# Performance work log

Hardware: AMD Instinct MI355X
Metric: run time of the kernel (lower is better)

Reference implementation:

```python
import jax, jax.numpy as jnp
import numpy as np

N_NODES = 100000
D_IN = 256
D_OUT = 128
N_EDGES = 1600000


def setup_inputs() -> dict:
    key = jax.random.key(0)
    k1, k2, k3, k4 = jax.random.split(key, 4)
    x = jax.random.normal(k1, (N_NODES, D_IN), dtype=jnp.float32)
    edge_index = jax.random.randint(k2, (2, N_EDGES), 0, N_NODES, dtype=jnp.int64)
    # GCNConv parameters (glorot-style scale)
    W = jax.random.normal(k3, (D_IN, D_OUT), dtype=jnp.float32) * (1.0 / np.sqrt(D_IN))
    b = jax.random.normal(k4, (D_OUT,), dtype=jnp.float32) * 0.01
    return {"x": x, "edge_index": edge_index, "W": W, "b": b}


def reference(x, edge_index, W, b):
    n = x.shape[0]
    # add self-loops (PyG GCNConv default)
    loop = jnp.arange(n, dtype=edge_index.dtype)
    src = jnp.concatenate([edge_index[0], loop])
    dst = jnp.concatenate([edge_index[1], loop])
    # symmetric normalization: deg^-1/2[src] * deg^-1/2[dst]
    ones = jnp.ones(src.shape[0], dtype=x.dtype)
    deg = jax.ops.segment_sum(ones, dst, num_segments=n)
    dinv = jnp.where(deg > 0, jax.lax.rsqrt(deg), 0.0)
    norm = dinv[src] * dinv[dst]  # [E+N]
    # linear transform at nodes, then gather-scale-scatter over edges
    h = x @ W  # [N, d_out]
    msg = h[src] * norm[:, None]  # [E+N, d_out]
    out = jax.ops.segment_sum(msg, dst, num_segments=n) + b
    # CRD.forward: relu then dropout (identity in eval mode)
    return jax.nn.relu(out)
```

## Files before the change

kernel.cpp:

```cpp
#include <hip/hip_runtime.h>
#include <stdint.h>

#define D_IN 256
#define D_OUT 128
#define MAXB 800
#define NCHUNK 256

typedef __attribute__((ext_vector_type(8))) short bf16x8;
typedef __attribute__((ext_vector_type(4))) float f32x4;

__device__ __forceinline__ unsigned short f2bf(float f) {
  union { float f; uint32_t u; } v; v.f = f;
  uint32_t u = v.u;
  uint32_t r = (u + 0x7FFFu + ((u >> 16) & 1u)) >> 16;
  return (unsigned short)r;
}
__device__ __forceinline__ float bf_lo(uint32_t u) {
  union { uint32_t u; float f; } v; v.u = u << 16; return v.f;
}
__device__ __forceinline__ float bf_hi(uint32_t u) {
  union { uint32_t u; float f; } v; v.u = u & 0xFFFF0000u; return v.f;
}

__global__ __launch_bounds__(256) void k_conv_w(const float* __restrict__ W,
                                                unsigned short* __restrict__ wt) {
  int idx = blockIdx.x * 256 + threadIdx.x;
  int n = idx >> 8;
  int k = idx & 255;
  wt[idx] = f2bf(W[k * D_OUT + n]);
}

__global__ __launch_bounds__(512) void k_gemm(const float* __restrict__ x,
                                              const unsigned short* __restrict__ wt,
                                              unsigned short* __restrict__ hp, int N) {
  int wave = threadIdx.x >> 6;
  int lane = threadIdx.x & 63;
  int m = lane & 15;
  int q = lane >> 4;

  bf16x8 bw[8];
  const unsigned short* wrow = wt + (size_t)(wave * 16 + m) * D_IN + q * 8;
#pragma unroll
  for (int kt = 0; kt < 8; ++kt)
    bw[kt] = *reinterpret_cast<const bf16x8*>(wrow + kt * 32);

  int tiles = (N + 15) >> 4;
  for (int t = blockIdx.x; t < tiles; t += gridDim.x) {
    int r0 = t * 16;
    const float* xrow = x + (size_t)(r0 + m) * D_IN + q * 8;

    f32x4 acc = {0.f, 0.f, 0.f, 0.f};
#pragma unroll
    for (int kt = 0; kt < 8; ++kt) {
      float4 u0 = *reinterpret_cast<const float4*>(xrow + kt * 32);
      float4 u1 = *reinterpret_cast<const float4*>(xrow + kt * 32 + 4);
      bf16x8 av;
      av[0] = (short)f2bf(u0.x); av[1] = (short)f2bf(u0.y);
      av[2] = (short)f2bf(u0.z); av[3] = (short)f2bf(u0.w);
      av[4] = (short)f2bf(u1.x); av[5] = (short)f2bf(u1.y);
      av[6] = (short)f2bf(u1.z); av[7] = (short)f2bf(u1.w);
      acc = __builtin_amdgcn_mfma_f32_16x16x32_bf16(av, bw[kt], acc, 0, 0, 0);
    }
#pragma unroll
    for (int r = 0; r < 4; ++r) {
      int row = r0 + q * 4 + r;
      hp[(size_t)row * D_OUT + wave * 16 + m] = f2bf(acc[r]);
    }
  }
}

__global__ __launch_bounds__(256) void k_passA(const int* __restrict__ ei, int E, int CH,
                                               int NB, int* __restrict__ cntm) {
  __shared__ int bins[MAXB];
  int c = blockIdx.x;
  for (int b = threadIdx.x; b < NB; b += 256) bins[b] = 0;
  __syncthreads();
  int start = c * CH, end = min(E, start + CH);
  for (int eb = start + (int)threadIdx.x * 4; eb < end; eb += 1024) {
    int kmax = end - eb; if (kmax > 4) kmax = 4;
    if (kmax == 4) {
      int4 v = *reinterpret_cast<const int4*>(ei + E + eb);
      atomicAdd(&bins[v.x >> 7], 1);
      atomicAdd(&bins[v.y >> 7], 1);
      atomicAdd(&bins[v.z >> 7], 1);
      atomicAdd(&bins[v.w >> 7], 1);
    } else {
      for (int k = 0; k < kmax; ++k) atomicAdd(&bins[ei[E + eb + k] >> 7], 1);
    }
  }
  __syncthreads();
  for (int b = threadIdx.x; b < NB; b += 256) cntm[(size_t)b * NCHUNK + c] = bins[b];
}

__global__ __launch_bounds__(NCHUNK) void k_scanB1(const int* __restrict__ cntm,
                                                   int* __restrict__ ofs,
                                                   int* __restrict__ tot) {
  __shared__ int sc[NCHUNK];
  int b = blockIdx.x, t = threadIdx.x;
  int v = cntm[(size_t)b * NCHUNK + t];
  sc[t] = v;
  __syncthreads();
  for (int off = 1; off < NCHUNK; off <<= 1) {
    int val = (t >= off) ? sc[t - off] : 0;
    __syncthreads();
    sc[t] += val;
    __syncthreads();
  }
  ofs[(size_t)b * NCHUNK + t] = sc[t] - v;
  if (t == NCHUNK - 1) tot[b] = sc[t];
}

__global__ __launch_bounds__(256) void k_scanB2(const int* __restrict__ tot,
                                                int* __restrict__ base, int NB,
                                                int* __restrict__ nptr, int N, int E) {
  __shared__ int sc[256];
  int t = threadIdx.x;
  int v[4];
  int s = 0;
#pragma unroll
  for (int j = 0; j < 4; ++j) {
    int i = t * 4 + j;
    v[j] = (i < NB) ? tot[i] : 0;
    s += v[j];
  }
  sc[t] = s;
  __syncthreads();
  for (int off = 1; off < 256; off <<= 1) {
    int val = (t >= off) ? sc[t - off] : 0;
    __syncthreads();
    sc[t] += val;
    __syncthreads();
  }
  int ex = sc[t] - s;
#pragma unroll
  for (int j = 0; j < 4; ++j) {
    int i = t * 4 + j;
    if (i < NB) base[i] = ex;
    ex += v[j];
  }
  if (t == 0) nptr[N] = E;
}

__global__ __launch_bounds__(256) void k_passC(const int* __restrict__ ei, int E, int CH,
                                               int NB, const int* __restrict__ ofs,
                                               const int* __restrict__ base,
                                               int* __restrict__ P) {
  __shared__ int cur[MAXB];
  int c = blockIdx.x;
  for (int b = threadIdx.x; b < NB; b += 256)
    cur[b] = base[b] + ofs[(size_t)b * NCHUNK + c];
  __syncthreads();
  int start = c * CH, end = min(E, start + CH);
  for (int eb = start + (int)threadIdx.x * 4; eb < end; eb += 1024) {
    int kmax = end - eb; if (kmax > 4) kmax = 4;
    int s4[4], d4[4];
    if (kmax == 4) {
      int4 vs = *reinterpret_cast<const int4*>(ei + eb);
      int4 vd = *reinterpret_cast<const int4*>(ei + E + eb);
      s4[0] = vs.x; s4[1] = vs.y; s4[2] = vs.z; s4[3] = vs.w;
      d4[0] = vd.x; d4[1] = vd.y; d4[2] = vd.z; d4[3] = vd.w;
    } else {
      for (int k = 0; k < kmax; ++k) { s4[k] = ei[eb + k]; d4[k] = ei[E + eb + k]; }
    }
#pragma unroll
    for (int k = 0; k < 4; ++k) {
      if (k >= kmax) break;
      int d = d4[k];
      int p = atomicAdd(&cur[d >> 7], 1);
      P[p] = s4[k] | ((d & 127) << 17);
    }
  }
}

__global__ __launch_bounds__(256) void k_sortd(const int* __restrict__ P,
                                               const int* __restrict__ base,
                                               const int* __restrict__ tot,
                                               int* __restrict__ nptr,
                                               float* __restrict__ dinv,
                                               int* __restrict__ P2, int N) {
  __shared__ int ideg[128];
  __shared__ int sc[128];
  __shared__ int cur[128];
  int b = blockIdx.x, t = threadIdx.x;
  if (t < 128) ideg[t] = 0;
  __syncthreads();
  int s0 = base[b], T = tot[b];
  for (int i = s0 + t; i < s0 + T; i += 256) atomicAdd(&ideg[P[i] >> 17], 1);
  __syncthreads();
  if (t < 128) sc[t] = ideg[t];
  __syncthreads();
  for (int off = 1; off < 128; off <<= 1) {
    int v = (t < 128 && t >= off) ? sc[t - off] : 0;
    __syncthreads();
    if (t < 128) sc[t] += v;
    __syncthreads();
  }
  if (t < 128) {
    int exc = s0 + sc[t] - ideg[t];
    int node = b * 128 + t;
    if (node < N) {
      nptr[node] = exc;
      dinv[node] = rsqrtf(1.0f + (float)ideg[t]);
    }
    cur[t] = exc;
  }
  __syncthreads();
  for (int i = s0 + t; i < s0 + T; i += 256) {
    int pk = P[i];
    int p = atomicAdd(&cur[pk >> 17], 1);
    P2[p] = pk & 0x1FFFF;
  }
}

__global__ __launch_bounds__(256) void k_agg(const int* __restrict__ P2,
                                             const int* __restrict__ nptr,
                                             const uint4* __restrict__ hrows,
                                             const float* __restrict__ dinv,
                                             const float* __restrict__ bias,
                                             float* __restrict__ out, int N) {
  int wave = threadIdx.x >> 6, lane = threadIdx.x & 63;
  int node = blockIdx.x * 4 + wave;
  if (node >= N) return;
  int rs = nptr[node], re = nptr[node + 1];
  int j = lane >> 4, c = lane & 15;

  float acc[8];
#pragma unroll
  for (int k = 0; k < 8; ++k) acc[k] = 0.f;

  for (int e = rs + j; e < re; e += 4) {
    int src = P2[e];
    float r = dinv[src];
    uint4 u = hrows[(size_t)src * 16 + c];
    acc[0] += r * bf_lo(u.x); acc[1] += r * bf_hi(u.x);
    acc[2] += r * bf_lo(u.y); acc[3] += r * bf_hi(u.y);
    acc[4] += r * bf_lo(u.z); acc[5] += r * bf_hi(u.z);
    acc[6] += r * bf_lo(u.w); acc[7] += r * bf_hi(u.w);
  }
#pragma unroll
  for (int k = 0; k < 8; ++k) {
    acc[k] += __shfl_xor(acc[k], 16);
    acc[k] += __shfl_xor(acc[k], 32);
  }
  if (j == 0) {
    float rsn = dinv[node];
    uint4 uh = hrows[(size_t)node * 16 + c];
    float self[8] = {bf_lo(uh.x), bf_hi(uh.x), bf_lo(uh.y), bf_hi(uh.y),
                     bf_lo(uh.z), bf_hi(uh.z), bf_lo(uh.w), bf_hi(uh.w)};
    const float4* b4 = reinterpret_cast<const float4*>(bias);
    float4 b0 = b4[c * 2], b1 = b4[c * 2 + 1];
    float bb[8] = {b0.x, b0.y, b0.z, b0.w, b1.x, b1.y, b1.z, b1.w};
    float o[8];
#pragma unroll
    for (int k = 0; k < 8; ++k) {
      float v = rsn * (acc[k] + rsn * self[k]) + bb[k];
      o[k] = v > 0.f ? v : 0.f;
    }
    float4* orow = reinterpret_cast<float4*>(out + (size_t)node * D_OUT + c * 8);
    orow[0] = float4{o[0], o[1], o[2], o[3]};
    orow[1] = float4{o[4], o[5], o[6], o[7]};
  }
}

extern "C" void kernel_launch(void* const* d_in, const int* in_sizes, int n_in,
                              void* d_out, int out_size, void* d_ws, size_t ws_size,
                              hipStream_t stream) {
  const float* x = (const float*)d_in[0];
  const int* ei = (const int*)d_in[1];
  const float* W = (const float*)d_in[2];
  const float* bias = (const float*)d_in[3];
  int N = in_sizes[0] / D_IN;
  int E = in_sizes[1] / 2;
  float* out = (float*)d_out;

  int NB = (N + 127) >> 7;
  int CH = ((E + NCHUNK - 1) / NCHUNK + 3) & ~3;

  char* w = (char*)d_ws;
  size_t off = 0;
  auto alloc = [&](size_t bytes) -> void* {
    void* p = w + off;
    off = (off + bytes + 255) & ~(size_t)255;
    return p;
  };
  unsigned short* wt = (unsigned short*)alloc((size_t)D_IN * D_OUT * 2);
  unsigned short* hp = (unsigned short*)alloc((size_t)N * D_OUT * 2);
  float* dinv = (float*)alloc((size_t)N * 4);
  int* cntm = (int*)alloc((size_t)NB * NCHUNK * 4);
  int* ofs = (int*)alloc((size_t)NB * NCHUNK * 4);
  int* tot = (int*)alloc((size_t)NB * 4);
  int* base = (int*)alloc((size_t)NB * 4);
  int* nptr = (int*)alloc((size_t)(N + 1) * 4);
  int* P = (int*)alloc((size_t)E * 4);
  int* P2 = (int*)alloc((size_t)E * 4);
  (void)ws_size; (void)n_in; (void)out_size;

  int tiles = (N + 15) >> 4;
  int gblocks = tiles < 512 ? tiles : 512;

  k_conv_w<<<(D_IN * D_OUT) / 256, 256, 0, stream>>>(W, wt);
  k_gemm<<<gblocks, 512, 0, stream>>>(x, wt, hp, N);
  k_passA<<<NCHUNK, 256, 0, stream>>>(ei, E, CH, NB, cntm);
  k_scanB1<<<NB, NCHUNK, 0, stream>>>(cntm, ofs, tot);
  k_scanB2<<<1, 256, 0, stream>>>(tot, base, NB, nptr, N, E);
  k_passC<<<NCHUNK, 256, 0, stream>>>(ei, E, CH, NB, ofs, base, P);
  k_sortd<<<NB, 256, 0, stream>>>(P, base, tot, nptr, dinv, P2, N);
  k_agg<<<(N + 3) / 4, 256, 0, stream>>>(P2, nptr, (const uint4*)hp, dinv, bias, out, N);
}
```

Measured before the change: 352.9 us.

## Double-buffer x tiles into LDS via async global_load_lds in GEMM

The GEMM kernel now stages each 16-row x tile into shared memory using direct global-to-LDS DMA loads with an XOR swizzle, double-buffering so the next tile loads while the current one is computed. Each block processes a contiguous range of tiles instead of grid-striding, and the grid size doubles to 1024 blocks. This is meant to hide global memory latency of the x read and spread it across more blocks. It adds 32KB LDS per block and a barrier per tile, which may limit occupancy.

```diff
diff --git a/kernel.cpp b/kernel.cpp
--- a/kernel.cpp
+++ b/kernel.cpp
@@ -20,6 +20,12 @@
 }
 __device__ __forceinline__ float bf_hi(uint32_t u) {
   union { uint32_t u; float f; } v; v.u = u & 0xFFFF0000u; return v.f;
+}
+
+__device__ __forceinline__ void dma16(const float* gsrc, float* ldst) {
+  __builtin_amdgcn_global_load_lds(
+      (const __attribute__((address_space(1))) void*)gsrc,
+      (__attribute__((address_space(3))) void*)ldst, 16, 0, 0);
 }
 
 __global__ __launch_bounds__(256) void k_conv_w(const float* __restrict__ W,
@@ -33,6 +39,8 @@
 __global__ __launch_bounds__(512) void k_gemm(const float* __restrict__ x,
                                               const unsigned short* __restrict__ wt,
                                               unsigned short* __restrict__ hp, int N) {
+  __shared__ float xl[2][16][256];
+
   int wave = threadIdx.x >> 6;
   int lane = threadIdx.x & 63;
   int m = lane & 15;
@@ -45,15 +53,37 @@
     bw[kt] = *reinterpret_cast<const bf16x8*>(wrow + kt * 32);
 
   int tiles = (N + 15) >> 4;
-  for (int t = blockIdx.x; t < tiles; t += gridDim.x) {
-    int r0 = t * 16;
-    const float* xrow = x + (size_t)(r0 + m) * D_IN + q * 8;
-
+  int ipb = (tiles + gridDim.x - 1) / gridDim.x;
+  int t0 = blockIdx.x * ipb;
+  int tend = t0 + ipb;
+  if (tend > tiles) tend = tiles;
+  if (t0 >= tend) return;
+
+  auto stage_tile = [&](int buf, int tt) {
+#pragma unroll
+    for (int rr = 0; rr < 2; ++rr) {
+      int r = wave + rr * 8;
+      const float* gsrc = x + ((size_t)tt * 16 + r) * D_IN + ((lane ^ (r & 7)) << 2);
+      dma16(gsrc, &xl[buf][r][0]);
+    }
+  };
+
+  stage_tile(0, t0);
+  __syncthreads();
+
+  int cur = 0;
+  int sw = m & 7;
+
+  for (int t = t0; t < tend; ++t) {
+    if (t + 1 < tend) stage_tile(cur ^ 1, t + 1);
+
+    const float* prow = &xl[cur][m][0];
     f32x4 acc = {0.f, 0.f, 0.f, 0.f};
 #pragma unroll
     for (int kt = 0; kt < 8; ++kt) {
-      float4 u0 = *reinterpret_cast<const float4*>(xrow + kt * 32);
-      float4 u1 = *reinterpret_cast<const float4*>(xrow + kt * 32 + 4);
+      int g0 = q * 2 + kt * 8;
+      float4 u0 = *reinterpret_cast<const float4*>(prow + ((g0 ^ sw) << 2));
+      float4 u1 = *reinterpret_cast<const float4*>(prow + (((g0 + 1) ^ sw) << 2));
       bf16x8 av;
       av[0] = (short)f2bf(u0.x); av[1] = (short)f2bf(u0.y);
       av[2] = (short)f2bf(u0.z); av[3] = (short)f2bf(u0.w);
@@ -61,11 +91,16 @@
       av[6] = (short)f2bf(u1.z); av[7] = (short)f2bf(u1.w);
       acc = __builtin_amdgcn_mfma_f32_16x16x32_bf16(av, bw[kt], acc, 0, 0, 0);
     }
+
+    int r0 = t * 16;
 #pragma unroll
     for (int r = 0; r < 4; ++r) {
       int row = r0 + q * 4 + r;
       hp[(size_t)row * D_OUT + wave * 16 + m] = f2bf(acc[r]);
     }
+
+    __syncthreads();
+    cur ^= 1;
   }
 }
 
@@ -296,7 +331,7 @@
   (void)ws_size; (void)n_in; (void)out_size;
 
   int tiles = (N + 15) >> 4;
-  int gblocks = tiles < 512 ? tiles : 512;
+  int gblocks = tiles < 1024 ? tiles : 1024;
 
   k_conv_w<<<(D_IN * D_OUT) / 256, 256, 0, stream>>>(W, wt);
   k_gemm<<<gblocks, 512, 0, stream>>>(x, wt, hp, N);
```

After: 304.1 us. 13.8% less time.
